# Kernel tuning notes

Measured on AMD Instinct MI355X. Metric: run time of the kernel, lower is better.

Reference implementation:

```python
import jax, jax.numpy as jnp
import numpy as np

B, L, N, F, H, HOR = 32, 12, 1024, 2, 128, 12


def setup_inputs() -> dict:
    key = jax.random.key(0)
    ks = jax.random.split(key, 9)
    x = jax.random.normal(ks[0], (B, L, N, F), dtype=jnp.float32)
    # A_phys: sparse-ish binary physical adjacency, then normalize_adj: add self-loops, row-normalize
    A_phys = (jax.random.uniform(ks[1], (N, N)) < 0.05).astype(jnp.float32)
    A = A_phys + jnp.eye(N, dtype=jnp.float32)
    A = A / (A.sum(axis=1, keepdims=True) + 1e-6)
    # GraphGRUCell params (single layer): lin_x: F -> 3H, lin_h: H -> 3H
    sx = 1.0 / np.sqrt(F)
    sh = 1.0 / np.sqrt(H)
    W_x = jax.random.uniform(ks[2], (F, 3 * H), minval=-sx, maxval=sx)
    b_x = jax.random.uniform(ks[3], (3 * H,), minval=-sx, maxval=sx)
    W_h = jax.random.uniform(ks[4], (H, 3 * H), minval=-sh, maxval=sh)
    b_h = jax.random.uniform(ks[5], (3 * H,), minval=-sh, maxval=sh)
    # head: H -> horizon
    W_head = jax.random.uniform(ks[6], (H, HOR), minval=-sh, maxval=sh)
    b_head = jax.random.uniform(ks[7], (HOR,), minval=-sh, maxval=sh)
    return {"x": x, "A": A, "W_x": W_x, "b_x": b_x, "W_h": W_h, "b_h": b_h,
            "W_head": W_head, "b_head": b_head}


def reference(x, A, W_x, b_x, W_h, b_h, W_head, b_head):
    Bv, Lv, Nv, Fv = x.shape
    Hv = W_h.shape[0]

    def step(h, xt):
        # graph aggregation of hidden state: [N,N] x [B,N,H] -> [B,N,H]
        Ah = jnp.einsum('ij,bjh->bih', A, h)
        x_gates = xt @ W_x + b_x          # [B,N,3H]
        h_gates = Ah @ W_h + b_h          # [B,N,3H]
        z_x, r_x, n_x = jnp.split(x_gates, 3, axis=-1)
        z_h, r_h, n_h = jnp.split(h_gates, 3, axis=-1)
        z = jax.nn.sigmoid(z_x + z_h)
        r = jax.nn.sigmoid(r_x + r_h)
        n = jnp.tanh(n_x + r * n_h)
        h_new = (1.0 - z) * n + z * h
        return h_new, None

    h0 = jnp.zeros((Bv, Nv, Hv), dtype=x.dtype)
    xs = jnp.moveaxis(x, 1, 0)  # [L,B,N,F]
    h, _ = jax.lax.scan(step, h0, xs)
    y = (h @ W_head + b_head).transpose(0, 2, 1)  # [B, horizon, N]
    return y
```

## Files before the change

### kernel.cpp

```cpp
#include <hip/hip_runtime.h>
#include <hip/hip_bf16.h>

#define BB 32
#define LL 12
#define NN 1024
#define HH 128
#define HORN 12
#define G3 384

typedef unsigned short u16;
typedef unsigned int u32;
typedef unsigned long long u64;
typedef __attribute__((ext_vector_type(8))) short short8;
typedef __attribute__((ext_vector_type(4))) float f32x4;

__device__ __forceinline__ u16 to_bf16(float f) {
    return __builtin_bit_cast(u16, __float2bfloat16(f));
}
__device__ __forceinline__ float bf_to_f(u32 bits) {
    return __builtin_bit_cast(float, bits << 16);
}
__device__ __forceinline__ void gl16(const u16* g, char* l) {
    __builtin_amdgcn_global_load_lds((const __attribute__((address_space(1))) u32*)g,
                                     (__attribute__((address_space(3))) u32*)l, 16, 0, 0);
}

__global__ void prep_abf(const float* __restrict__ A, u16* __restrict__ Abf) {
    int t = blockIdx.x * blockDim.x + threadIdx.x;
    float4 v = ((const float4*)A)[t];
    ushort4 o;
    o.x = to_bf16(v.x); o.y = to_bf16(v.y); o.z = to_bf16(v.z); o.w = to_bf16(v.w);
    ((ushort4*)Abf)[t] = o;
}

__global__ void prep_whT(const float* __restrict__ W_h, u16* __restrict__ whT) {
    int t = blockIdx.x * blockDim.x + threadIdx.x;
    if (t >= HH * G3) return;
    int c = t / HH, k = t % HH;
    whT[c * HH + k] = to_bf16(W_h[k * G3 + c]);
}

template <bool FIRST, bool LAST>
__global__ __launch_bounds__(256, 2) void gru_step(
    const u16* __restrict__ Abf, const u16* __restrict__ hT_old,
    u16* __restrict__ hT_new, const u16* __restrict__ whT,
    const float* __restrict__ x, const float* __restrict__ W_x,
    const float* __restrict__ b_x, const float* __restrict__ b_h,
    const float* __restrict__ W_head, const float* __restrict__ b_head,
    float* __restrict__ out, int t) {
    __shared__ __align__(16) char smem[73728];

    int bid = blockIdx.x;
    int swz = (bid & 7) * 64 + (bid >> 3);
    int b = swz >> 4;
    int i0 = (swz & 15) * 64;
    int tid = threadIdx.x;
    int w = tid >> 6, lane = tid & 63;
    int lcol = lane & 15, kgrp = lane >> 4;
    int wm = w >> 1, wn = w & 1;
    u32 swzl = (u32)((lcol & 7) << 4);
    u32 a_b = (u32)((wm * 32 + lcol) * 128);
    u32 b_b = (u32)(8192 + (wn * 64 + lcol) * 128);

    f32x4 acc[2][4];
#pragma unroll
    for (int m = 0; m < 2; ++m)
#pragma unroll
        for (int n = 0; n < 4; ++n) acc[m][n] = (f32x4){0.f, 0.f, 0.f, 0.f};
    u64 hreg[2][4] = {{0, 0, 0, 0}, {0, 0, 0, 0}};

    if (!FIRST) {
        int lr3 = lane >> 3, lc8 = lane & 7;
        const u16* ag[2]; u32 al[2];
        const u16* bg[4]; u32 bl[4];
#pragma unroll
        for (int q = 0; q < 2; ++q) {
            int r = w * 16 + q * 8 + lr3;
            ag[q] = Abf + (size_t)(i0 + r) * 1024 + (lc8 ^ (r & 7)) * 8;
            al[q] = (u32)(w * 2048 + q * 1024);
        }
#pragma unroll
        for (int q = 0; q < 4; ++q) {
            int r = w * 32 + q * 8 + lr3;
            bg[q] = hT_old + (size_t)b * 131072 + (size_t)r * 1024 + (lc8 ^ (r & 7)) * 8;
            bl[q] = (u32)(8192 + w * 4096 + q * 1024);
        }

#pragma unroll
        for (int pc = 0; pc < 3; ++pc) {
            int o = pc * 64;
            char* base = smem + pc * 24576;
#pragma unroll
            for (int q = 0; q < 2; ++q) gl16(ag[q] + o, base + al[q]);
#pragma unroll
            for (int q = 0; q < 4; ++q) gl16(bg[q] + o, base + bl[q]);
        }

        int cstar = i0 >> 6;
        u32 sb = 0;
        for (int c = 0; c < 16; ++c) {
            if (c < 14)      asm volatile("s_waitcnt vmcnt(12)" ::: "memory");
            else if (c < 15) asm volatile("s_waitcnt vmcnt(6)" ::: "memory");
            else             asm volatile("s_waitcnt vmcnt(0)" ::: "memory");
            __builtin_amdgcn_s_barrier();
            __builtin_amdgcn_sched_barrier(0);

            if (c == cstar) {
#pragma unroll
                for (int sub = 0; sub < 2; ++sub) {
                    int hh = w * 32 + sub * 16 + lcol;
                    u32 rb = sb + 8192u + (u32)(hh * 128);
                    u32 sw = (u32)((hh & 7) << 4);
#pragma unroll
                    for (int rt = 0; rt < 4; ++rt)
                        hreg[sub][rt] = *(const u64*)(smem + rb + (((u32)(rt * 32 + kgrp * 8)) ^ sw));
                }
                asm volatile("s_waitcnt lgkmcnt(0)" ::: "memory");
                __builtin_amdgcn_sched_barrier(0);
            }

            __builtin_amdgcn_s_setprio(1);
#pragma unroll
            for (int ks = 0; ks < 2; ++ks) {
                u32 kb = ((u32)(ks * 64 + kgrp * 16)) ^ swzl;
                short8 a0 = *(const short8*)(smem + sb + a_b + kb);
                short8 a1 = *(const short8*)(smem + sb + a_b + 2048 + kb);
                short8 b0 = *(const short8*)(smem + sb + b_b + kb);
                short8 b1 = *(const short8*)(smem + sb + b_b + 2048 + kb);
                short8 b2 = *(const short8*)(smem + sb + b_b + 4096 + kb);
                short8 b3 = *(const short8*)(smem + sb + b_b + 6144 + kb);
                acc[0][0] = __builtin_amdgcn_mfma_f32_16x16x32_bf16(a0, b0, acc[0][0], 0, 0, 0);
                acc[0][1] = __builtin_amdgcn_mfma_f32_16x16x32_bf16(a0, b1, acc[0][1], 0, 0, 0);
                acc[0][2] = __builtin_amdgcn_mfma_f32_16x16x32_bf16(a0, b2, acc[0][2], 0, 0, 0);
                acc[0][3] = __builtin_amdgcn_mfma_f32_16x16x32_bf16(a0, b3, acc[0][3], 0, 0, 0);
                acc[1][0] = __builtin_amdgcn_mfma_f32_16x16x32_bf16(a1, b0, acc[1][0], 0, 0, 0);
                acc[1][1] = __builtin_amdgcn_mfma_f32_16x16x32_bf16(a1, b1, acc[1][1], 0, 0, 0);
                acc[1][2] = __builtin_amdgcn_mfma_f32_16x16x32_bf16(a1, b2, acc[1][2], 0, 0, 0);
                acc[1][3] = __builtin_amdgcn_mfma_f32_16x16x32_bf16(a1, b3, acc[1][3], 0, 0, 0);
            }
            __builtin_amdgcn_s_setprio(0);
            asm volatile("" ::: "memory");
            __builtin_amdgcn_s_barrier();
            if (c < 13) {
                int o = (c + 3) * 64;
#pragma unroll
                for (int q = 0; q < 2; ++q) gl16(ag[q] + o, smem + sb + al[q]);
#pragma unroll
                for (int q = 0; q < 4; ++q) gl16(bg[q] + o, smem + sb + bl[q]);
            }
            sb = (sb == 49152u) ? 0u : sb + 24576u;
        }
        asm volatile("" ::: "memory");
        __builtin_amdgcn_s_barrier();
    }

#pragma unroll
    for (int m = 0; m < 2; ++m)
#pragma unroll
        for (int n = 0; n < 4; ++n)
#pragma unroll
            for (int ri = 0; ri < 4; ++ri) {
                int row = wm * 32 + m * 16 + kgrp * 4 + ri;
                int col = wn * 64 + n * 16 + lcol;
                *(u16*)(smem + row * 256 + (((u32)(2 * col)) ^ ((u32)(row & 7) << 4))) =
                    to_bf16(acc[m][n][ri]);
            }
    __syncthreads();

#pragma unroll
    for (int sub = 0; sub < 2; ++sub) {
        int hh = w * 32 + sub * 16 + lcol;
        short8 bw[3][4];
#pragma unroll
        for (int g = 0; g < 3; ++g)
#pragma unroll
            for (int ks = 0; ks < 4; ++ks)
                bw[g][ks] = *(const short8*)(whT + (size_t)(g * 128 + hh) * 128 + ks * 32 + kgrp * 8);

        f32x4 acc2[4][3];
#pragma unroll
        for (int rt = 0; rt < 4; ++rt)
#pragma unroll
            for (int g = 0; g < 3; ++g) acc2[rt][g] = (f32x4){0.f, 0.f, 0.f, 0.f};

        __builtin_amdgcn_s_setprio(1);
#pragma unroll
        for (int rt = 0; rt < 4; ++rt) {
            u32 ab2 = (u32)((rt * 16 + lcol) * 256);
#pragma unroll
            for (int ks = 0; ks < 4; ++ks) {
                short8 a2 = *(const short8*)(smem + ab2 + (((u32)(ks * 64 + kgrp * 16)) ^ swzl));
                acc2[rt][0] = __builtin_amdgcn_mfma_f32_16x16x32_bf16(a2, bw[0][ks], acc2[rt][0], 0, 0, 0);
                acc2[rt][1] = __builtin_amdgcn_mfma_f32_16x16x32_bf16(a2, bw[1][ks], acc2[rt][1], 0, 0, 0);
                acc2[rt][2] = __builtin_amdgcn_mfma_f32_16x16x32_bf16(a2, bw[2][ks], acc2[rt][2], 0, 0, 0);
            }
        }
        __builtin_amdgcn_s_setprio(0);

        float bxz = b_x[hh], bxr = b_x[128 + hh], bxn = b_x[256 + hh];
        float bhz = b_h[hh], bhr = b_h[128 + hh], bhn = b_h[256 + hh];
        float wx0z = W_x[hh], wx0r = W_x[128 + hh], wx0n = W_x[256 + hh];
        float wx1z = W_x[G3 + hh], wx1r = W_x[G3 + 128 + hh], wx1n = W_x[G3 + 256 + hh];
#pragma unroll
        for (int rt = 0; rt < 4; ++rt) {
            u64 h4 = hreg[sub][rt];
#pragma unroll
            for (int ri = 0; ri < 4; ++ri) {
                int rl = rt * 16 + kgrp * 4 + ri;
                int i = i0 + rl;
                const float* xp = x + ((size_t)(b * LL + t) * NN + i) * 2;
                float x0 = xp[0], x1 = xp[1];
                float zin = acc2[rt][0][ri] + bhz + fmaf(x0, wx0z, fmaf(x1, wx1z, bxz));
                float rin = acc2[rt][1][ri] + bhr + fmaf(x0, wx0r, fmaf(x1, wx1r, bxr));
                float z = 1.f / (1.f + __expf(-zin));
                float rg = 1.f / (1.f + __expf(-rin));
                float nin = fmaf(rg, acc2[rt][2][ri] + bhn, fmaf(x0, wx0n, fmaf(x1, wx1n, bxn)));
                nin = fmaxf(nin, -40.f);
                float e = __expf(-2.f * nin);
                float n = (1.f - e) / (1.f + e);
                float hold = bf_to_f((u32)((h4 >> (16 * ri)) & 0xffffu));
                float hv = fmaf(z, hold - n, n);
                *(u16*)(smem + 16384 + hh * 128 + (((u32)(2 * rl)) ^ ((u32)(hh & 7) << 4))) = to_bf16(hv);
            }
        }
    }
    __syncthreads();

    if (!LAST) {
#pragma unroll
        for (int c2 = 0; c2 < 4; ++c2) {
            int o = c2 * 4096 + tid * 16;
            int nr = o >> 7, cb = o & 127;
            uint4 v = *(const uint4*)(smem + 16384 + nr * 128 + (((u32)cb) ^ ((u32)(nr & 7) << 4)));
            *(uint4*)((char*)(hT_new + (size_t)b * 131072 + (size_t)nr * 1024 + i0) + cb) = v;
        }
    } else {
        float* wl = (float*)(smem + 32768);
        float* blh = (float*)(smem + 38912);
        for (int ix = tid; ix < HH * HORN; ix += 256) wl[ix] = W_head[ix];
        if (tid < HORN) blh[tid] = b_head[tid];
        __syncthreads();
        int il = tid & 63, hg = tid >> 6;
        float a0 = blh[hg], a1 = blh[hg + 4], a2 = blh[hg + 8];
        for (int hh = 0; hh < 128; ++hh) {
            float hv = bf_to_f((u32)*(const u16*)(smem + 16384 + hh * 128 + (((u32)(2 * il)) ^ ((u32)(hh & 7) << 4))));
            a0 = fmaf(hv, wl[hh * HORN + hg], a0);
            a1 = fmaf(hv, wl[hh * HORN + hg + 4], a1);
            a2 = fmaf(hv, wl[hh * HORN + hg + 8], a2);
        }
        out[(size_t)(b * HORN + hg) * NN + i0 + il] = a0;
        out[(size_t)(b * HORN + hg + 4) * NN + i0 + il] = a1;
        out[(size_t)(b * HORN + hg + 8) * NN + i0 + il] = a2;
    }
}

extern "C" void kernel_launch(void* const* d_in, const int* in_sizes, int n_in,
                              void* d_out, int out_size, void* d_ws, size_t ws_size,
                              hipStream_t stream) {
    const float* x = (const float*)d_in[0];
    const float* A = (const float*)d_in[1];
    const float* W_x = (const float*)d_in[2];
    const float* b_x = (const float*)d_in[3];
    const float* W_h = (const float*)d_in[4];
    const float* b_h = (const float*)d_in[5];
    const float* W_head = (const float*)d_in[6];
    const float* b_head = (const float*)d_in[7];
    float* out = (float*)d_out;
    char* ws = (char*)d_ws;

    u16* hT0 = (u16*)(ws + 0);
    u16* hT1 = (u16*)(ws + 8388608);
    u16* Abf = (u16*)(ws + 16777216);
    u16* whT = (u16*)(ws + 18874368);

    prep_abf<<<1024, 256, 0, stream>>>(A, Abf);
    prep_whT<<<(HH * G3 + 255) / 256, 256, 0, stream>>>(W_h, whT);

    gru_step<true, false><<<512, 256, 0, stream>>>(Abf, hT1, hT0, whT, x, W_x, b_x, b_h,
                                                   W_head, b_head, out, 0);
    u16* hTo = hT0; u16* hTn = hT1;
    for (int t = 1; t < LL - 1; ++t) {
        gru_step<false, false><<<512, 256, 0, stream>>>(Abf, hTo, hTn, whT, x, W_x, b_x, b_h,
                                                        W_head, b_head, out, t);
        u16* tmp = hTo; hTo = hTn; hTn = tmp;
    }
    gru_step<false, true><<<512, 256, 0, stream>>>(Abf, hTo, hTn, whT, x, W_x, b_x, b_h,
                                                   W_head, b_head, out, LL - 1);
}
```

Before: 295.5 us.

## Give each wave private LDS tiles to remove per-chunk block barriers

After: 390.3 us. 32.1% more time.

```diff
diff --git a/kernel.cpp b/kernel.cpp
--- a/kernel.cpp
+++ b/kernel.cpp
@@ -58,9 +58,7 @@
     int w = tid >> 6, lane = tid & 63;
     int lcol = lane & 15, kgrp = lane >> 4;
     int wm = w >> 1, wn = w & 1;
-    u32 swzl = (u32)((lcol & 7) << 4);
-    u32 a_b = (u32)((wm * 32 + lcol) * 128);
-    u32 b_b = (u32)(8192 + (wn * 64 + lcol) * 128);
+    int hq = wn * 2 + wm;
 
     f32x4 acc[2][4];
 #pragma unroll
@@ -70,89 +68,98 @@
     u64 hreg[2][4] = {{0, 0, 0, 0}, {0, 0, 0, 0}};
 
     if (!FIRST) {
-        int lr3 = lane >> 3, lc8 = lane & 7;
-        const u16* ag[2]; u32 al[2];
-        const u16* bg[4]; u32 bl[4];
+        int lr2 = lane >> 2, lq = lane & 3;
+        u32 gsw = (u32)((lq ^ (lr2 & 3)) * 8);
+        const u16* agl[2]; u32 al[2];
+        const u16* bgl[4]; u32 bl[4];
 #pragma unroll
         for (int q = 0; q < 2; ++q) {
-            int r = w * 16 + q * 8 + lr3;
-            ag[q] = Abf + (size_t)(i0 + r) * 1024 + (lc8 ^ (r & 7)) * 8;
-            al[q] = (u32)(w * 2048 + q * 1024);
+            agl[q] = Abf + (size_t)(i0 + wm * 32 + q * 16 + lr2) * 1024 + gsw;
+            al[q] = (u32)(w * 6144 + q * 1024);
         }
 #pragma unroll
         for (int q = 0; q < 4; ++q) {
-            int r = w * 32 + q * 8 + lr3;
-            bg[q] = hT_old + (size_t)b * 131072 + (size_t)r * 1024 + (lc8 ^ (r & 7)) * 8;
-            bl[q] = (u32)(8192 + w * 4096 + q * 1024);
+            bgl[q] = hT_old + (size_t)b * 131072 + (size_t)(wn * 64 + q * 16 + lr2) * 1024 + gsw;
+            bl[q] = (u32)(w * 6144 + 2048 + q * 1024);
         }
 
 #pragma unroll
         for (int pc = 0; pc < 3; ++pc) {
-            int o = pc * 64;
             char* base = smem + pc * 24576;
-#pragma unroll
-            for (int q = 0; q < 2; ++q) gl16(ag[q] + o, base + al[q]);
-#pragma unroll
-            for (int q = 0; q < 4; ++q) gl16(bg[q] + o, base + bl[q]);
-        }
-
-        int cstar = i0 >> 6;
+            int o = pc * 32;
+#pragma unroll
+            for (int q = 0; q < 2; ++q) gl16(agl[q] + o, base + al[q]);
+#pragma unroll
+            for (int q = 0; q < 4; ++q) gl16(bgl[q] + o, base + bl[q]);
+        }
+
+        int c0 = i0 >> 5;
+        u32 fsw = (u32)((kgrp ^ (lcol & 3)) * 16);
         u32 sb = 0;
-        for (int c = 0; c < 16; ++c) {
-            if (c < 14)      asm volatile("s_waitcnt vmcnt(12)" ::: "memory");
-            else if (c < 15) asm volatile("s_waitcnt vmcnt(6)" ::: "memory");
+        for (int c = 0; c < 32; ++c) {
+            if (c < 30)      asm volatile("s_waitcnt vmcnt(12)" ::: "memory");
+            else if (c < 31) asm volatile("s_waitcnt vmcnt(6)" ::: "memory");
             else             asm volatile("s_waitcnt vmcnt(0)" ::: "memory");
-            __builtin_amdgcn_s_barrier();
             __builtin_amdgcn_sched_barrier(0);
 
-            if (c == cstar) {
+            u32 wbase = sb + (u32)(w * 6144);
+            short8 a0 = *(const short8*)(smem + wbase + (u32)(lcol * 64) + fsw);
+            short8 a1 = *(const short8*)(smem + wbase + (u32)((16 + lcol) * 64) + fsw);
+            short8 b0 = *(const short8*)(smem + wbase + 2048 + (u32)(lcol * 64) + fsw);
+            short8 b1 = *(const short8*)(smem + wbase + 2048 + (u32)((16 + lcol) * 64) + fsw);
+            short8 b2 = *(const short8*)(smem + wbase + 2048 + (u32)((32 + lcol) * 64) + fsw);
+            short8 b3 = *(const short8*)(smem + wbase + 2048 + (u32)((48 + lcol) * 64) + fsw);
+            __builtin_amdgcn_s_setprio(1);
+            acc[0][0] = __builtin_amdgcn_mfma_f32_16x16x32_bf16(a0, b0, acc[0][0], 0, 0, 0);
+            acc[0][1] = __builtin_amdgcn_mfma_f32_16x16x32_bf16(a0, b1, acc[0][1], 0, 0, 0);
+            acc[0][2] = __builtin_amdgcn_mfma_f32_16x16x32_bf16(a0, b2, acc[0][2], 0, 0, 0);
+            acc[0][3] = __builtin_amdgcn_mfma_f32_16x16x32_bf16(a0, b3, acc[0][3], 0, 0, 0);
+            acc[1][0] = __builtin_amdgcn_mfma_f32_16x16x32_bf16(a1, b0, acc[1][0], 0, 0, 0);
+            acc[1][1] = __builtin_amdgcn_mfma_f32_16x16x32_bf16(a1, b1, acc[1][1], 0, 0, 0);
+            acc[1][2] = __builtin_amdgcn_mfma_f32_16x16x32_bf16(a1, b2, acc[1][2], 0, 0, 0);
+            acc[1][3] = __builtin_amdgcn_mfma_f32_16x16x32_bf16(a1, b3, acc[1][3], 0, 0, 0);
+            __builtin_amdgcn_s_setprio(0);
+
+            if (c == c0) {
 #pragma unroll
                 for (int sub = 0; sub < 2; ++sub) {
-                    int hh = w * 32 + sub * 16 + lcol;
-                    u32 rb = sb + 8192u + (u32)(hh * 128);
-                    u32 sw = (u32)((hh & 7) << 4);
-#pragma unroll
-                    for (int rt = 0; rt < 4; ++rt)
-                        hreg[sub][rt] = *(const u64*)(smem + rb + (((u32)(rt * 32 + kgrp * 8)) ^ sw));
+                    int nloc = wm * 32 + sub * 16 + lcol;
+                    u32 rb = sb + (u32)(w * 6144 + 2048 + nloc * 64);
+                    u32 nsw = (u32)(nloc & 3);
+#pragma unroll
+                    for (int rt = 0; rt < 2; ++rt) {
+                        u32 g = (u32)(rt * 2 + (kgrp >> 1));
+                        hreg[sub][rt] = *(const u64*)(smem + rb + ((g ^ nsw) * 16) + (u32)((kgrp & 1) * 8));
+                    }
                 }
-                asm volatile("s_waitcnt lgkmcnt(0)" ::: "memory");
-                __builtin_amdgcn_sched_barrier(0);
-            }
-
-            __builtin_amdgcn_s_setprio(1);
-#pragma unroll
-            for (int ks = 0; ks < 2; ++ks) {
-                u32 kb = ((u32)(ks * 64 + kgrp * 16)) ^ swzl;
-                short8 a0 = *(const short8*)(smem + sb + a_b + kb);
-                short8 a1 = *(const short8*)(smem + sb + a_b + 2048 + kb);
-                short8 b0 = *(const short8*)(smem + sb + b_b + kb);
-                short8 b1 = *(const short8*)(smem + sb + b_b + 2048 + kb);
-                short8 b2 = *(const short8*)(smem + sb + b_b + 4096 + kb);
-                short8 b3 = *(const short8*)(smem + sb + b_b + 6144 + kb);
-                acc[0][0] = __builtin_amdgcn_mfma_f32_16x16x32_bf16(a0, b0, acc[0][0], 0, 0, 0);
-                acc[0][1] = __builtin_amdgcn_mfma_f32_16x16x32_bf16(a0, b1, acc[0][1], 0, 0, 0);
-                acc[0][2] = __builtin_amdgcn_mfma_f32_16x16x32_bf16(a0, b2, acc[0][2], 0, 0, 0);
-                acc[0][3] = __builtin_amdgcn_mfma_f32_16x16x32_bf16(a0, b3, acc[0][3], 0, 0, 0);
-                acc[1][0] = __builtin_amdgcn_mfma_f32_16x16x32_bf16(a1, b0, acc[1][0], 0, 0, 0);
-                acc[1][1] = __builtin_amdgcn_mfma_f32_16x16x32_bf16(a1, b1, acc[1][1], 0, 0, 0);
-                acc[1][2] = __builtin_amdgcn_mfma_f32_16x16x32_bf16(a1, b2, acc[1][2], 0, 0, 0);
-                acc[1][3] = __builtin_amdgcn_mfma_f32_16x16x32_bf16(a1, b3, acc[1][3], 0, 0, 0);
-            }
-            __builtin_amdgcn_s_setprio(0);
-            asm volatile("" ::: "memory");
-            __builtin_amdgcn_s_barrier();
-            if (c < 13) {
-                int o = (c + 3) * 64;
-#pragma unroll
-                for (int q = 0; q < 2; ++q) gl16(ag[q] + o, smem + sb + al[q]);
-#pragma unroll
-                for (int q = 0; q < 4; ++q) gl16(bg[q] + o, smem + sb + bl[q]);
+            }
+            if (c == c0 + 1) {
+#pragma unroll
+                for (int sub = 0; sub < 2; ++sub) {
+                    int nloc = wm * 32 + sub * 16 + lcol;
+                    u32 rb = sb + (u32)(w * 6144 + 2048 + nloc * 64);
+                    u32 nsw = (u32)(nloc & 3);
+#pragma unroll
+                    for (int rt = 2; rt < 4; ++rt) {
+                        u32 g = (u32)((rt - 2) * 2 + (kgrp >> 1));
+                        hreg[sub][rt] = *(const u64*)(smem + rb + ((g ^ nsw) * 16) + (u32)((kgrp & 1) * 8));
+                    }
+                }
+            }
+
+            asm volatile("s_waitcnt lgkmcnt(0)" ::: "memory");
+            __builtin_amdgcn_sched_barrier(0);
+            if (c < 29) {
+                int o = (c + 3) * 32;
+#pragma unroll
+                for (int q = 0; q < 2; ++q) gl16(agl[q] + o, smem + sb + al[q]);
+#pragma unroll
+                for (int q = 0; q < 4; ++q) gl16(bgl[q] + o, smem + sb + bl[q]);
             }
             sb = (sb == 49152u) ? 0u : sb + 24576u;
         }
-        asm volatile("" ::: "memory");
-        __builtin_amdgcn_s_barrier();
-    }
+    }
+    __syncthreads();
 
 #pragma unroll
     for (int m = 0; m < 2; ++m)
@@ -167,9 +174,10 @@
             }
     __syncthreads();
 
+    u32 swzl = (u32)((lcol & 7) << 4);
 #pragma unroll
     for (int sub = 0; sub < 2; ++sub) {
-        int hh = w * 32 + sub * 16 + lcol;
+        int hh = hq * 32 + sub * 16 + lcol;
         short8 bw[3][4];
 #pragma unroll
         for (int g = 0; g < 3; ++g)
```
